# Performance work log

Measured on AMD Instinct MI355X. Metric: run time of the kernel, lower is better.

Reference implementation:

```python
import jax, jax.numpy as jnp
import numpy as np

B, T, C = 2, 2048, 1024
R = 16
LORA_SCALE = 1.0 / R  # lora_alpha(=1) / r


def lora_linear(x, w, b, a, bb):
    # loralib: y = x @ W^T + bias + (x @ A^T) @ B^T * scaling
    return x @ w.T + b + (x @ a.T) @ bb.T * LORA_SCALE


def setup_inputs() -> dict:
    key = jax.random.key(0)
    ks = jax.random.split(key, 8)
    s = 0.02
    return {
        "x": jax.random.normal(ks[0], (B, T, C), jnp.float32),
        "w_attn": jax.random.normal(ks[1], (3 * C, C), jnp.float32) * s,
        "b_attn": jnp.zeros((3 * C,), jnp.float32),
        "lora_a_attn": jax.random.normal(ks[2], (R, C), jnp.float32) * s,
        "lora_b_attn": jnp.zeros((3 * C, R), jnp.float32),
        "w_proj": jax.random.normal(ks[3], (C, C), jnp.float32) * s,
        "b_proj": jnp.zeros((C,), jnp.float32),
        "lora_a_proj": jax.random.normal(ks[4], (R, C), jnp.float32) * s,
        "lora_b_proj": jnp.zeros((C, R), jnp.float32),
        "n_head": 16,
    }


def reference(x, w_attn, b_attn, lora_a_attn, lora_b_attn, w_proj, b_proj,
              lora_a_proj, lora_b_proj, n_head):
    b, t, c = x.shape
    hd = c // n_head
    qkv = lora_linear(x, w_attn, b_attn, lora_a_attn, lora_b_attn)
    q, k, v = jnp.split(qkv, 3, axis=2)
    # (B, H, T, hd)
    q = q.reshape(b, t, n_head, hd).transpose(0, 2, 1, 3)
    k = k.reshape(b, t, n_head, hd).transpose(0, 2, 1, 3)
    v = v.reshape(b, t, n_head, hd).transpose(0, 2, 1, 3)
    att = jnp.einsum("bhqd,bhkd->bhqk", q, k) * (1.0 / np.sqrt(hd).astype(np.float32))
    causal = jnp.tril(jnp.ones((t, t), bool))
    att = jnp.where(causal[None, None], att, jnp.float32(-jnp.inf))
    att = jax.nn.softmax(att, axis=-1)
    y = jnp.einsum("bhqk,bhkd->bhqd", att, v)
    y = y.transpose(0, 2, 1, 3).reshape(b, t, c)
    return lora_linear(y, w_proj, b_proj, lora_a_proj, lora_b_proj)
```

## Files before the change

### kernel.cpp

```cpp
#include <hip/hip_runtime.h>

typedef __attribute__((ext_vector_type(8))) short bf16x8;
typedef __attribute__((ext_vector_type(4))) float f32x4;

__device__ __forceinline__ float bf2f(unsigned short u) {
    unsigned int x = ((unsigned int)u) << 16;
    float f;
    __builtin_memcpy(&f, &x, 4);
    return f;
}
__device__ __forceinline__ unsigned short f2bf(float f) {
    unsigned int x;
    __builtin_memcpy(&x, &f, 4);
    x += 0x7FFFu + ((x >> 16) & 1u);
    return (unsigned short)(x >> 16);
}

#define GLOAD_LDS16(gp, lp)                                      \
    __builtin_amdgcn_global_load_lds(                            \
        (const __attribute__((address_space(1))) void*)(gp),     \
        (__attribute__((address_space(3))) void*)(lp), 16, 0, 0)

__global__ __launch_bounds__(256) void cast_f32_bf16(
    const float* __restrict__ in, unsigned short* __restrict__ out, int n) {
    int i = (blockIdx.x * 256 + threadIdx.x) * 4;
    if (i >= n) return;
    float4 v = *(const float4*)(in + i);
    out[i + 0] = f2bf(v.x);
    out[i + 1] = f2bf(v.y);
    out[i + 2] = f2bf(v.z);
    out[i + 3] = f2bf(v.w);
}

__global__ __launch_bounds__(256) void fold_lora(
    const float* __restrict__ W, const float* __restrict__ Ain,
    const float* __restrict__ Bin, unsigned short* __restrict__ Weff, int NK) {
    int idx = blockIdx.x * 256 + threadIdx.x;
    if (idx >= NK) return;
    int n = idx >> 10;
    int k = idx & 1023;
    float s = 0.f;
#pragma unroll
    for (int r = 0; r < 16; ++r)
        s += Bin[n * 16 + r] * Ain[r * 1024 + k];
    Weff[idx] = f2bf(W[idx] + 0.0625f * s);
}

template <bool F32OUT>
__global__ __launch_bounds__(256) void gemm_bt_bias(
    const unsigned short* __restrict__ A, const unsigned short* __restrict__ B,
    const float* __restrict__ bias, unsigned short* __restrict__ Cb,
    float* __restrict__ Cf, int M, int N, int K) {
    __shared__ unsigned short sA[128 * 32];
    __shared__ unsigned short sB[128 * 32];
    const int tid = threadIdx.x;
    const int wave = tid >> 6, lane = tid & 63;
    const int quad = lane >> 4, l16 = lane & 15;
    const int m0 = blockIdx.y * 128, n0 = blockIdx.x * 128;
    const int wm = (wave & 1) * 64, wn = (wave >> 1) * 64;

    const int srow = wave * 32 + (lane >> 2);
    const int scol = (lane & 3) * 8;
    const unsigned short* Ag = A + (size_t)(m0 + srow) * K + scol;
    const unsigned short* Bg = B + (size_t)(n0 + srow) * K + scol;
    unsigned short* sAw = sA + wave * 1024;
    unsigned short* sBw = sB + wave * 1024;
    const size_t kjump = (size_t)16 * K;

    f32x4 acc[4][4];
#pragma unroll
    for (int i = 0; i < 4; ++i)
#pragma unroll
        for (int j = 0; j < 4; ++j) acc[i][j] = (f32x4){0.f, 0.f, 0.f, 0.f};

    for (int k0 = 0; k0 < K; k0 += 32) {
        __syncthreads();
        GLOAD_LDS16(Ag + k0, sAw);
        GLOAD_LDS16(Ag + k0 + kjump, sAw + 512);
        GLOAD_LDS16(Bg + k0, sBw);
        GLOAD_LDS16(Bg + k0 + kjump, sBw + 512);
        __syncthreads();
        bf16x8 af[4], bfr[4];
#pragma unroll
        for (int mi = 0; mi < 4; ++mi)
            af[mi] = *(const bf16x8*)&sA[(wm + mi * 16 + l16) * 32 + quad * 8];
#pragma unroll
        for (int ni = 0; ni < 4; ++ni)
            bfr[ni] = *(const bf16x8*)&sB[(wn + ni * 16 + l16) * 32 + quad * 8];
#pragma unroll
        for (int mi = 0; mi < 4; ++mi)
#pragma unroll
            for (int ni = 0; ni < 4; ++ni)
                acc[mi][ni] = __builtin_amdgcn_mfma_f32_16x16x32_bf16(
                    af[mi], bfr[ni], acc[mi][ni], 0, 0, 0);
    }
    float bv[4];
#pragma unroll
    for (int ni = 0; ni < 4; ++ni) bv[ni] = bias[n0 + wn + ni * 16 + l16];
#pragma unroll
    for (int mi = 0; mi < 4; ++mi)
#pragma unroll
        for (int ni = 0; ni < 4; ++ni)
#pragma unroll
            for (int r = 0; r < 4; ++r) {
                int row = m0 + wm + mi * 16 + quad * 4 + r;
                int col = n0 + wn + ni * 16 + l16;
                float val = acc[mi][ni][r] + bv[ni];
                if (F32OUT)
                    Cf[(size_t)row * N + col] = val;
                else
                    Cb[(size_t)row * N + col] = f2bf(val);
            }
}

__global__ __launch_bounds__(256) void transpose_v(
    const unsigned short* __restrict__ qkv, unsigned short* __restrict__ Vt) {
    const int b = blockIdx.z, h = blockIdx.y, t0 = blockIdx.x * 64;
    __shared__ unsigned short tile[64][68];
    const int tid = threadIdx.x;
    const int r = tid >> 3, c8 = (tid & 7) * 8;
    const unsigned short* src = qkv + (size_t)(b * 2048) * 3072 + 2048 + h * 64;
#pragma unroll
    for (int p = 0; p < 2; ++p) {
        int t = p * 32 + r;
        const unsigned short* s = src + (size_t)(t0 + t) * 3072 + c8;
#pragma unroll
        for (int j = 0; j < 8; ++j) tile[t][c8 + j] = s[j];
    }
    __syncthreads();
    unsigned short* dst = Vt + (size_t)((b * 16 + h) * 64) * 2048;
#pragma unroll
    for (int p = 0; p < 2; ++p) {
        int d = p * 32 + r;
        unsigned short* o = dst + (size_t)d * 2048 + t0 + c8;
#pragma unroll
        for (int j = 0; j < 8; ++j) o[j] = tile[c8 + j][d];
    }
}

__global__ __launch_bounds__(256) void attn_kernel(
    const unsigned short* __restrict__ qkv,
    const unsigned short* __restrict__ Vt,
    unsigned short* __restrict__ y) {
    const int b = blockIdx.z, h = blockIdx.y;
    const int bh = b * 16 + h;
    const int qblk = (int)blockIdx.x ^ (((bh >> 3) & 1) ? 31 : 0);
    const int w = threadIdx.x >> 6, lane = threadIdx.x & 63;
    const int quad = lane >> 4, l16 = lane & 15;
    const int q0 = qblk * 64 + w * 16;
    const int ntiles = qblk + 1;

    __shared__ unsigned short sK[64 * 72];
    __shared__ unsigned short sV[64 * 72];
    __shared__ unsigned short sP[4][16 * 72];

    const unsigned short* Qb = qkv + (size_t)(b * 2048) * 3072 + h * 64;
    const unsigned short* Kg = Qb + 1024;
    const unsigned short* Vg = Vt + (size_t)(bh * 64) * 2048;

    const int rlo = threadIdx.x >> 3;
    const int c8 = (threadIdx.x & 7) * 8;

    bf16x8 qf0 = *(const bf16x8*)(Qb + (size_t)(q0 + l16) * 3072 + quad * 8);
    bf16x8 qf1 = *(const bf16x8*)(Qb + (size_t)(q0 + l16) * 3072 + 32 + quad * 8);

    f32x4 o[4];
    float lacc[4];
#pragma unroll
    for (int nt = 0; nt < 4; ++nt) o[nt] = (f32x4){0.f, 0.f, 0.f, 0.f};
#pragma unroll
    for (int r = 0; r < 4; ++r) lacc[r] = 0.f;

    const float csc = 0.125f * 1.44269504088896340736f;

    bf16x8 kr0 = *(const bf16x8*)(Kg + (size_t)rlo * 3072 + c8);
    bf16x8 kr1 = *(const bf16x8*)(Kg + (size_t)(rlo + 32) * 3072 + c8);
    bf16x8 vr0 = *(const bf16x8*)(Vg + (size_t)rlo * 2048 + c8);
    bf16x8 vr1 = *(const bf16x8*)(Vg + (size_t)(rlo + 32) * 2048 + c8);

    for (int it = 0; it < ntiles; ++it) {
        const int kv0 = it * 64;
        __syncthreads();
        *(bf16x8*)&sK[rlo * 72 + c8] = kr0;
        *(bf16x8*)&sK[(rlo + 32) * 72 + c8] = kr1;
        *(bf16x8*)&sV[rlo * 72 + c8] = vr0;
        *(bf16x8*)&sV[(rlo + 32) * 72 + c8] = vr1;
        if (it + 1 < ntiles) {
            const int nx = kv0 + 64;
            kr0 = *(const bf16x8*)(Kg + (size_t)(nx + rlo) * 3072 + c8);
            kr1 = *(const bf16x8*)(Kg + (size_t)(nx + rlo + 32) * 3072 + c8);
            vr0 = *(const bf16x8*)(Vg + (size_t)rlo * 2048 + nx + c8);
            vr1 = *(const bf16x8*)(Vg + (size_t)(rlo + 32) * 2048 + nx + c8);
        }
        __syncthreads();

        f32x4 S[4];
#pragma unroll
        for (int f = 0; f < 4; ++f) {
            bf16x8 klo = *(const bf16x8*)&sK[(f * 16 + l16) * 72 + quad * 8];
            bf16x8 khi = *(const bf16x8*)&sK[(f * 16 + l16) * 72 + 32 + quad * 8];
            S[f] = (f32x4){0.f, 0.f, 0.f, 0.f};
            S[f] = __builtin_amdgcn_mfma_f32_16x16x32_bf16(qf0, klo, S[f], 0, 0, 0);
            S[f] = __builtin_amdgcn_mfma_f32_16x16x32_bf16(qf1, khi, S[f], 0, 0, 0);
        }
        if (it == qblk) {
#pragma unroll
            for (int f = 0; f < 4; ++f)
#pragma unroll
                for (int r = 0; r < 4; ++r) {
                    int col = kv0 + f * 16 + l16;
                    int qr = q0 + quad * 4 + r;
                    float p = (col <= qr) ? exp2f(S[f][r] * csc) : 0.f;
                    lacc[r] += p;
                    sP[w][(quad * 4 + r) * 72 + f * 16 + l16] = f2bf(p);
                }
        } else {
#pragma unroll
            for (int f = 0; f < 4; ++f)
#pragma unroll
                for (int r = 0; r < 4; ++r) {
                    float p = exp2f(S[f][r] * csc);
                    lacc[r] += p;
                    sP[w][(quad * 4 + r) * 72 + f * 16 + l16] = f2bf(p);
                }
        }
        asm volatile("" ::: "memory");
        bf16x8 pf0 = *(const bf16x8*)&sP[w][l16 * 72 + quad * 8];
        bf16x8 pf1 = *(const bf16x8*)&sP[w][l16 * 72 + 32 + quad * 8];
#pragma unroll
        for (int nt = 0; nt < 4; ++nt) {
            bf16x8 v0 = *(const bf16x8*)&sV[(nt * 16 + l16) * 72 + quad * 8];
            bf16x8 v1 = *(const bf16x8*)&sV[(nt * 16 + l16) * 72 + 32 + quad * 8];
            o[nt] = __builtin_amdgcn_mfma_f32_16x16x32_bf16(pf0, v0, o[nt], 0, 0, 0);
            o[nt] = __builtin_amdgcn_mfma_f32_16x16x32_bf16(pf1, v1, o[nt], 0, 0, 0);
        }
    }

    float lt[4];
#pragma unroll
    for (int r = 0; r < 4; ++r) lt[r] = lacc[r];
#pragma unroll
    for (int d = 1; d < 16; d <<= 1)
#pragma unroll
        for (int r = 0; r < 4; ++r) lt[r] += __shfl_xor(lt[r], d);

    unsigned short* yb = y + (size_t)(b * 2048) * 1024 + h * 64;
#pragma unroll
    for (int nt = 0; nt < 4; ++nt)
#pragma unroll
        for (int r = 0; r < 4; ++r)
            yb[(size_t)(q0 + quad * 4 + r) * 1024 + nt * 16 + l16] =
                f2bf(o[nt][r] / lt[r]);
}

extern "C" void kernel_launch(void* const* d_in, const int* in_sizes, int n_in,
                              void* d_out, int out_size, void* d_ws, size_t ws_size,
                              hipStream_t stream) {
    const float* x       = (const float*)d_in[0];
    const float* w_attn  = (const float*)d_in[1];
    const float* b_attn  = (const float*)d_in[2];
    const float* la_attn = (const float*)d_in[3];
    const float* lb_attn = (const float*)d_in[4];
    const float* w_proj  = (const float*)d_in[5];
    const float* b_proj  = (const float*)d_in[6];
    const float* la_proj = (const float*)d_in[7];
    const float* lb_proj = (const float*)d_in[8];
    float* out = (float*)d_out;

    char* w = (char*)d_ws;
    unsigned short* xb        = (unsigned short*)w; w += (size_t)4096 * 1024 * 2;
    unsigned short* Weff_attn = (unsigned short*)w; w += (size_t)3072 * 1024 * 2;
    unsigned short* Weff_proj = (unsigned short*)w; w += (size_t)1024 * 1024 * 2;
    unsigned short* qkv       = (unsigned short*)w; w += (size_t)4096 * 3072 * 2;
    unsigned short* Vt        = (unsigned short*)w; w += (size_t)32 * 64 * 2048 * 2;
    unsigned short* y         = (unsigned short*)w; w += (size_t)4096 * 1024 * 2;

    cast_f32_bf16<<<4096, 256, 0, stream>>>(x, xb, 4096 * 1024);
    fold_lora<<<(3072 * 1024) / 256, 256, 0, stream>>>(w_attn, la_attn, lb_attn,
                                                       Weff_attn, 3072 * 1024);
    fold_lora<<<(1024 * 1024) / 256, 256, 0, stream>>>(w_proj, la_proj, lb_proj,
                                                       Weff_proj, 1024 * 1024);
    gemm_bt_bias<false><<<dim3(24, 32), 256, 0, stream>>>(
        xb, Weff_attn, b_attn, qkv, (float*)nullptr, 4096, 3072, 1024);
    transpose_v<<<dim3(32, 16, 2), 256, 0, stream>>>(qkv, Vt);
    attn_kernel<<<dim3(32, 16, 2), 256, 0, stream>>>(qkv, Vt, y);
    gemm_bt_bias<true><<<dim3(8, 32), 256, 0, stream>>>(
        y, Weff_proj, b_proj, (unsigned short*)nullptr, out, 4096, 1024, 1024);
}
```

Measured before the change: 222.7 us.

## Split causal attention KV range into two partial blocks with a finalize pass

Each query block's causal KV tiles are split into two halves, so the partial-attention grid doubles and the largest query blocks are launched first. Each partial block writes unnormalized fp32 outputs and row sums to workspace. A new finalize kernel adds the two partials, divides by the combined sum and casts to bf16. This is meant to raise parallelism and shorten the longest per-block work, at the cost of a second launch and extra fp32 round-trip traffic through global memory.

Result: slower. 249.2 us (+11.9%).

```diff
diff --git a/kernel.cpp b/kernel.cpp
--- a/kernel.cpp
+++ b/kernel.cpp
@@ -138,17 +138,39 @@
     }
 }
 
-__global__ __launch_bounds__(256) void attn_kernel(
+__global__ __launch_bounds__(256) void attn_partial(
     const unsigned short* __restrict__ qkv,
     const unsigned short* __restrict__ Vt,
-    unsigned short* __restrict__ y) {
+    float* __restrict__ opart,
+    float* __restrict__ lpart) {
     const int b = blockIdx.z, h = blockIdx.y;
     const int bh = b * 16 + h;
-    const int qblk = (int)blockIdx.x ^ (((bh >> 3) & 1) ? 31 : 0);
+    const int idx = blockIdx.x;
+    const int qblk = 31 - (idx >> 1);
+    const int part = idx & 1;
     const int w = threadIdx.x >> 6, lane = threadIdx.x & 63;
     const int quad = lane >> 4, l16 = lane & 15;
     const int q0 = qblk * 64 + w * 16;
     const int ntiles = qblk + 1;
+    const int half = (ntiles + 1) >> 1;
+    const int lo = part ? half : 0;
+    const int hi = part ? ntiles : half;
+
+    float* op = opart + (size_t)part * 4096 * 1024;
+    float* lp = lpart + (size_t)part * 32 * 2048;
+    float* ob = op + (size_t)(b * 2048) * 1024 + h * 64;
+
+    if (lo >= hi) {
+#pragma unroll
+        for (int nt = 0; nt < 4; ++nt)
+#pragma unroll
+            for (int r = 0; r < 4; ++r)
+                ob[(size_t)(q0 + quad * 4 + r) * 1024 + nt * 16 + l16] = 0.f;
+        if (l16 == 0)
+#pragma unroll
+            for (int r = 0; r < 4; ++r) lp[bh * 2048 + q0 + quad * 4 + r] = 0.f;
+        return;
+    }
 
     __shared__ unsigned short sK[64 * 72];
     __shared__ unsigned short sV[64 * 72];
@@ -173,19 +195,20 @@
 
     const float csc = 0.125f * 1.44269504088896340736f;
 
-    bf16x8 kr0 = *(const bf16x8*)(Kg + (size_t)rlo * 3072 + c8);
-    bf16x8 kr1 = *(const bf16x8*)(Kg + (size_t)(rlo + 32) * 3072 + c8);
-    bf16x8 vr0 = *(const bf16x8*)(Vg + (size_t)rlo * 2048 + c8);
-    bf16x8 vr1 = *(const bf16x8*)(Vg + (size_t)(rlo + 32) * 2048 + c8);
-
-    for (int it = 0; it < ntiles; ++it) {
+    const int kvlo = lo * 64;
+    bf16x8 kr0 = *(const bf16x8*)(Kg + (size_t)(kvlo + rlo) * 3072 + c8);
+    bf16x8 kr1 = *(const bf16x8*)(Kg + (size_t)(kvlo + rlo + 32) * 3072 + c8);
+    bf16x8 vr0 = *(const bf16x8*)(Vg + (size_t)rlo * 2048 + kvlo + c8);
+    bf16x8 vr1 = *(const bf16x8*)(Vg + (size_t)(rlo + 32) * 2048 + kvlo + c8);
+
+    for (int it = lo; it < hi; ++it) {
         const int kv0 = it * 64;
         __syncthreads();
         *(bf16x8*)&sK[rlo * 72 + c8] = kr0;
         *(bf16x8*)&sK[(rlo + 32) * 72 + c8] = kr1;
         *(bf16x8*)&sV[rlo * 72 + c8] = vr0;
         *(bf16x8*)&sV[(rlo + 32) * 72 + c8] = vr1;
-        if (it + 1 < ntiles) {
+        if (it + 1 < hi) {
             const int nx = kv0 + 64;
             kr0 = *(const bf16x8*)(Kg + (size_t)(nx + rlo) * 3072 + c8);
             kr1 = *(const bf16x8*)(Kg + (size_t)(nx + rlo + 32) * 3072 + c8);
@@ -244,13 +267,32 @@
 #pragma unroll
         for (int r = 0; r < 4; ++r) lt[r] += __shfl_xor(lt[r], d);
 
-    unsigned short* yb = y + (size_t)(b * 2048) * 1024 + h * 64;
+    if (l16 == 0)
+#pragma unroll
+        for (int r = 0; r < 4; ++r) lp[bh * 2048 + q0 + quad * 4 + r] = lt[r];
 #pragma unroll
     for (int nt = 0; nt < 4; ++nt)
 #pragma unroll
         for (int r = 0; r < 4; ++r)
-            yb[(size_t)(q0 + quad * 4 + r) * 1024 + nt * 16 + l16] =
-                f2bf(o[nt][r] / lt[r]);
+            ob[(size_t)(q0 + quad * 4 + r) * 1024 + nt * 16 + l16] = o[nt][r];
+}
+
+__global__ __launch_bounds__(256) void attn_finalize(
+    const float* __restrict__ opart, const float* __restrict__ lpart,
+    unsigned short* __restrict__ y) {
+    int i = (blockIdx.x * 256 + threadIdx.x) * 4;
+    float4 a = *(const float4*)(opart + i);
+    float4 b4 = *(const float4*)(opart + (size_t)4096 * 1024 + i);
+    int row = i >> 10;
+    int c = i & 1023;
+    int bh = (row >> 11) * 16 + (c >> 6);
+    int q = row & 2047;
+    float l = lpart[bh * 2048 + q] + lpart[32 * 2048 + bh * 2048 + q];
+    float inv = 1.f / l;
+    y[i + 0] = f2bf((a.x + b4.x) * inv);
+    y[i + 1] = f2bf((a.y + b4.y) * inv);
+    y[i + 2] = f2bf((a.z + b4.z) * inv);
+    y[i + 3] = f2bf((a.w + b4.w) * inv);
 }
 
 extern "C" void kernel_launch(void* const* d_in, const int* in_sizes, int n_in,
@@ -274,6 +316,8 @@
     unsigned short* qkv       = (unsigned short*)w; w += (size_t)4096 * 3072 * 2;
     unsigned short* Vt        = (unsigned short*)w; w += (size_t)32 * 64 * 2048 * 2;
     unsigned short* y         = (unsigned short*)w; w += (size_t)4096 * 1024 * 2;
+    float* opart              = (float*)w;          w += (size_t)2 * 4096 * 1024 * 4;
+    float* lpart              = (float*)w;          w += (size_t)2 * 32 * 2048 * 4;
 
     cast_f32_bf16<<<4096, 256, 0, stream>>>(x, xb, 4096 * 1024);
     fold_lora<<<(3072 * 1024) / 256, 256, 0, stream>>>(w_attn, la_attn, lb_attn,
@@ -283,7 +327,8 @@
     gemm_bt_bias<false><<<dim3(24, 32), 256, 0, stream>>>(
         xb, Weff_attn, b_attn, qkv, (float*)nullptr, 4096, 3072, 1024);
     transpose_v<<<dim3(32, 16, 2), 256, 0, stream>>>(qkv, Vt);
-    attn_kernel<<<dim3(32, 16, 2), 256, 0, stream>>>(qkv, Vt, y);
+    attn_partial<<<dim3(64, 16, 2), 256, 0, stream>>>(qkv, Vt, opart, lpart);
+    attn_finalize<<<4096, 256, 0, stream>>>(opart, lpart, y);
     gemm_bt_bias<true><<<dim3(8, 32), 256, 0, stream>>>(
         y, Weff_proj, b_proj, (unsigned short*)nullptr, out, 4096, 1024, 1024);
 }
```

## Fuse prep kernels and transpose QK^T MFMA to simplify softmax row sums

Applied to the files above, without the earlier changes.

Merges the x cast and both LoRA-fold kernels into a single prep launch indexed by block range. In attention, swaps the MFMA operands so each lane holds one query row across four key columns. The row sum becomes a single scalar per lane, reduced with two shuffles instead of a 16-wide butterfly per row. P is packed with v_cvt_pk_bf16_f32 and exponentiated with raw v_exp_f32, writing 8-byte stores to LDS. This cuts launch overhead and softmax ALU/LDS instruction count, at the risk of subtle layout or masking errors.

Result: faster. 210.8 us (-5.3%).

```diff
diff --git a/kernel.cpp b/kernel.cpp
--- a/kernel.cpp
+++ b/kernel.cpp
@@ -21,22 +21,34 @@
         (const __attribute__((address_space(1))) void*)(gp),     \
         (__attribute__((address_space(3))) void*)(lp), 16, 0, 0)
 
-__global__ __launch_bounds__(256) void cast_f32_bf16(
-    const float* __restrict__ in, unsigned short* __restrict__ out, int n) {
-    int i = (blockIdx.x * 256 + threadIdx.x) * 4;
-    if (i >= n) return;
-    float4 v = *(const float4*)(in + i);
-    out[i + 0] = f2bf(v.x);
-    out[i + 1] = f2bf(v.y);
-    out[i + 2] = f2bf(v.z);
-    out[i + 3] = f2bf(v.w);
-}
-
-__global__ __launch_bounds__(256) void fold_lora(
-    const float* __restrict__ W, const float* __restrict__ Ain,
-    const float* __restrict__ Bin, unsigned short* __restrict__ Weff, int NK) {
-    int idx = blockIdx.x * 256 + threadIdx.x;
-    if (idx >= NK) return;
+__global__ __launch_bounds__(256) void prep(
+    const float* __restrict__ x, unsigned short* __restrict__ xb,
+    const float* __restrict__ w_attn, const float* __restrict__ la_attn,
+    const float* __restrict__ lb_attn, unsigned short* __restrict__ Weff_attn,
+    const float* __restrict__ w_proj, const float* __restrict__ la_proj,
+    const float* __restrict__ lb_proj, unsigned short* __restrict__ Weff_proj) {
+    const int bid = blockIdx.x;
+    if (bid < 4096) {
+        int i = (bid * 256 + threadIdx.x) * 4;
+        float4 v = *(const float4*)(x + i);
+        xb[i + 0] = f2bf(v.x);
+        xb[i + 1] = f2bf(v.y);
+        xb[i + 2] = f2bf(v.z);
+        xb[i + 3] = f2bf(v.w);
+        return;
+    }
+    const float* W;
+    const float* Ain;
+    const float* Bin;
+    unsigned short* Weff;
+    int idx;
+    if (bid < 16384) {
+        idx = (bid - 4096) * 256 + threadIdx.x;
+        W = w_attn; Ain = la_attn; Bin = lb_attn; Weff = Weff_attn;
+    } else {
+        idx = (bid - 16384) * 256 + threadIdx.x;
+        W = w_proj; Ain = la_proj; Bin = lb_proj; Weff = Weff_proj;
+    }
     int n = idx >> 10;
     int k = idx & 1023;
     float s = 0.f;
@@ -165,11 +177,9 @@
     bf16x8 qf1 = *(const bf16x8*)(Qb + (size_t)(q0 + l16) * 3072 + 32 + quad * 8);
 
     f32x4 o[4];
-    float lacc[4];
+    float lacc = 0.f;
 #pragma unroll
     for (int nt = 0; nt < 4; ++nt) o[nt] = (f32x4){0.f, 0.f, 0.f, 0.f};
-#pragma unroll
-    for (int r = 0; r < 4; ++r) lacc[r] = 0.f;
 
     const float csc = 0.125f * 1.44269504088896340736f;
 
@@ -200,29 +210,36 @@
             bf16x8 klo = *(const bf16x8*)&sK[(f * 16 + l16) * 72 + quad * 8];
             bf16x8 khi = *(const bf16x8*)&sK[(f * 16 + l16) * 72 + 32 + quad * 8];
             S[f] = (f32x4){0.f, 0.f, 0.f, 0.f};
-            S[f] = __builtin_amdgcn_mfma_f32_16x16x32_bf16(qf0, klo, S[f], 0, 0, 0);
-            S[f] = __builtin_amdgcn_mfma_f32_16x16x32_bf16(qf1, khi, S[f], 0, 0, 0);
+            S[f] = __builtin_amdgcn_mfma_f32_16x16x32_bf16(klo, qf0, S[f], 0, 0, 0);
+            S[f] = __builtin_amdgcn_mfma_f32_16x16x32_bf16(khi, qf1, S[f], 0, 0, 0);
         }
-        if (it == qblk) {
-#pragma unroll
-            for (int f = 0; f < 4; ++f)
-#pragma unroll
-                for (int r = 0; r < 4; ++r) {
-                    int col = kv0 + f * 16 + l16;
-                    int qr = q0 + quad * 4 + r;
-                    float p = (col <= qr) ? exp2f(S[f][r] * csc) : 0.f;
-                    lacc[r] += p;
-                    sP[w][(quad * 4 + r) * 72 + f * 16 + l16] = f2bf(p);
-                }
-        } else {
-#pragma unroll
-            for (int f = 0; f < 4; ++f)
-#pragma unroll
-                for (int r = 0; r < 4; ++r) {
-                    float p = exp2f(S[f][r] * csc);
-                    lacc[r] += p;
-                    sP[w][(quad * 4 + r) * 72 + f * 16 + l16] = f2bf(p);
-                }
+        const bool diag = (it == qblk);
+        const int qr16 = w * 16 + l16;
+#pragma unroll
+        for (int f = 0; f < 4; ++f) {
+            float p0, p1, p2, p3;
+            {
+                float sv = S[f][0] * csc;
+                asm("v_exp_f32 %0, %1" : "=v"(p0) : "v"(sv));
+                sv = S[f][1] * csc;
+                asm("v_exp_f32 %0, %1" : "=v"(p1) : "v"(sv));
+                sv = S[f][2] * csc;
+                asm("v_exp_f32 %0, %1" : "=v"(p2) : "v"(sv));
+                sv = S[f][3] * csc;
+                asm("v_exp_f32 %0, %1" : "=v"(p3) : "v"(sv));
+            }
+            if (diag) {
+                int c = f * 16 + quad * 4;
+                p0 = (c + 0 <= qr16) ? p0 : 0.f;
+                p1 = (c + 1 <= qr16) ? p1 : 0.f;
+                p2 = (c + 2 <= qr16) ? p2 : 0.f;
+                p3 = (c + 3 <= qr16) ? p3 : 0.f;
+            }
+            lacc += (p0 + p1) + (p2 + p3);
+            unsigned int d0, d1;
+            asm("v_cvt_pk_bf16_f32 %0, %1, %2" : "=v"(d0) : "v"(p0), "v"(p1));
+            asm("v_cvt_pk_bf16_f32 %0, %1, %2" : "=v"(d1) : "v"(p2), "v"(p3));
+            *(uint2*)&sP[w][l16 * 72 + f * 16 + quad * 4] = (uint2){d0, d1};
         }
         asm volatile("" ::: "memory");
         bf16x8 pf0 = *(const bf16x8*)&sP[w][l16 * 72 + quad * 8];
@@ -236,13 +253,11 @@
         }
     }
 
+    lacc += __shfl_xor(lacc, 16);
+    lacc += __shfl_xor(lacc, 32);
     float lt[4];
 #pragma unroll
-    for (int r = 0; r < 4; ++r) lt[r] = lacc[r];
-#pragma unroll
-    for (int d = 1; d < 16; d <<= 1)
-#pragma unroll
-        for (int r = 0; r < 4; ++r) lt[r] += __shfl_xor(lt[r], d);
+    for (int r = 0; r < 4; ++r) lt[r] = __shfl(lacc, quad * 4 + r);
 
     unsigned short* yb = y + (size_t)(b * 2048) * 1024 + h * 64;
 #pragma unroll
@@ -275,11 +290,8 @@
     unsigned short* Vt        = (unsigned short*)w; w += (size_t)32 * 64 * 2048 * 2;
     unsigned short* y         = (unsigned short*)w; w += (size_t)4096 * 1024 * 2;
 
-    cast_f32_bf16<<<4096, 256, 0, stream>>>(x, xb, 4096 * 1024);
-    fold_lora<<<(3072 * 1024) / 256, 256, 0, stream>>>(w_attn, la_attn, lb_attn,
-                                                       Weff_attn, 3072 * 1024);
-    fold_lora<<<(1024 * 1024) / 256, 256, 0, stream>>>(w_proj, la_proj, lb_proj,
-                                                       Weff_proj, 1024 * 1024);
+    prep<<<20480, 256, 0, stream>>>(x, xb, w_attn, la_attn, lb_attn, Weff_attn,
+                                    w_proj, la_proj, lb_proj, Weff_proj);
     gemm_bt_bias<false><<<dim3(24, 32), 256, 0, stream>>>(
         xb, Weff_attn, b_attn, qkv, (float*)nullptr, 4096, 3072, 1024);
     transpose_v<<<dim3(32, 16, 2), 256, 0, stream>>>(qkv, Vt);
```
